# Kernel tuning notes

Measured on AMD Instinct MI355X. Metric: run time of the kernel, lower is better.

The kernel has to match this reference:

```python
import jax, jax.numpy as jnp
import numpy as np

D_MODEL, D_STATE, D_CONV, EXPAND = 1024, 16, 4, 2
D_INNER = EXPAND * D_MODEL
BATCH, L = 2, 2048


def setup_inputs() -> dict:
    key = jax.random.key(0)
    ks = jax.random.split(key, 8)
    s = lambda fan: 1.0 / float(np.sqrt(fan))
    x = jax.random.normal(ks[0], (BATCH, L, D_MODEL), jnp.float32)
    W_in = jax.random.normal(ks[1], (D_MODEL, 2 * D_INNER), jnp.float32) * s(D_MODEL)
    conv_w = jax.random.normal(ks[2], (D_INNER, 1, D_CONV), jnp.float32) * s(D_CONV)
    conv_b = jax.random.normal(ks[3], (D_INNER,), jnp.float32) * 0.1
    W_x = jax.random.normal(ks[4], (D_INNER, 2 * D_STATE + 1), jnp.float32) * s(D_INNER)
    w_dt = jax.random.normal(ks[5], (D_INNER,), jnp.float32)
    b_dt = jax.random.normal(ks[6], (D_INNER,), jnp.float32) * 0.1
    W_out = jax.random.normal(ks[7], (D_INNER, D_MODEL), jnp.float32) * s(D_INNER)
    A_log = jnp.log(jnp.broadcast_to(jnp.arange(1, D_STATE + 1, dtype=jnp.float32), (D_INNER, D_STATE)))
    Dp = jnp.ones((D_INNER,), jnp.float32)
    return dict(x=x, W_in=W_in, conv_w=conv_w, conv_b=conv_b, W_x=W_x,
                w_dt=w_dt, b_dt=b_dt, A_log=A_log, Dp=Dp, W_out=W_out)


def _silu(v):
    return v * jax.nn.sigmoid(v)


def _forward(x, W_in, conv_w, conv_b, W_x, w_dt, b_dt, A_log, Dp, W_out):
    xz = x @ W_in                                   # (B,L,2*Di)
    x_, z = jnp.split(xz, 2, axis=-1)               # (B,L,Di) each
    # causal depthwise conv over length (== torch pad d_conv-1 both sides then [:L])
    xc = jnp.transpose(x_, (0, 2, 1))               # (B,Di,L)
    xc = jax.lax.conv_general_dilated(
        xc, conv_w, window_strides=(1,), padding=[(D_CONV - 1, 0)],
        dimension_numbers=('NCH', 'OIH', 'NCH'), feature_group_count=D_INNER)
    xc = xc + conv_b[None, :, None]
    x_ = _silu(jnp.transpose(xc, (0, 2, 1)))        # (B,L,Di)

    bcd = x_ @ W_x                                  # (B,L,2N+1)
    B_ = bcd[..., :D_STATE]                         # (B,L,N)
    C = bcd[..., D_STATE:2 * D_STATE]               # (B,L,N)
    dt = jax.nn.softplus(bcd[..., -1:] * w_dt + b_dt)  # (B,L,Di)
    A = -jnp.exp(A_log)                             # (Di,N)

    def step(h, inp):
        dt_t, B_t, C_t, x_t = inp                   # (B,Di),(B,N),(B,N),(B,Di)
        dA = jnp.exp(dt_t[..., None] * A)           # (B,Di,N)
        h = dA * h + (dt_t * x_t)[..., None] * B_t[:, None, :]
        y = jnp.einsum('bdn,bn->bd', h, C_t)
        return h, y

    h0 = jnp.zeros((x.shape[0], D_INNER, D_STATE), x.dtype)
    xs = (jnp.transpose(dt, (1, 0, 2)), jnp.transpose(B_, (1, 0, 2)),
          jnp.transpose(C, (1, 0, 2)), jnp.transpose(x_, (1, 0, 2)))
    _, ys = jax.lax.scan(step, h0, xs)              # ys: (L,B,Di)
    y = jnp.transpose(ys, (1, 0, 2)) + x_ * Dp      # skip connection via D
    return (y * _silu(z)) @ W_out                   # (B,L,d_model)


def reference(x, W_in, conv_w, conv_b, W_x, w_dt, b_dt, A_log, Dp, W_out):
    return _forward(x, W_in, conv_w, conv_b, W_x, w_dt, b_dt, A_log, Dp, W_out)
```

## Files before the change

### kernel.cpp

```cpp
#include <hip/hip_runtime.h>
#include <hip/hip_bf16.h>
#include <stdint.h>

#define D_MODEL 1024
#define D_STATE 16
#define D_CONV  4
#define D_INNER 2048
#define BATCH   2
#define SEQLEN  2048
#define NROWS   (BATCH*SEQLEN)
#define BCD_LD  36
#define NCHUNK  32
#define CHUNKLEN (SEQLEN/NCHUNK)
#define KS2     16
#define L2E 1.44269504088896340f

typedef __attribute__((ext_vector_type(8))) short   short8;
typedef __attribute__((ext_vector_type(4))) float   f32x4;

__device__ __forceinline__ uint16_t f2bf(float f) {
    uint32_t u = __float_as_uint(f);
    return (uint16_t)((u + 0x7FFFu + ((u >> 16) & 1u)) >> 16);
}
__device__ __forceinline__ void gload16(const uint16_t* g, uint16_t* l) {
    __builtin_amdgcn_global_load_lds(
        (const __attribute__((address_space(1))) void*)g,
        (__attribute__((address_space(3))) void*)l, 16, 0, 0);
}
__device__ __forceinline__ void gload16f(const float* g, float* l) {
    __builtin_amdgcn_global_load_lds(
        (const __attribute__((address_space(1))) void*)g,
        (__attribute__((address_space(3))) void*)l, 16, 0, 0);
}
__device__ __forceinline__ float softplus_f(float v) {
    return fmaxf(v, 0.f) + __logf(1.f + __expf(-fabsf(v)));
}
__device__ __forceinline__ float silu_f(float v) {
    return v / (1.f + __expf(-v));
}
__device__ __forceinline__ short8 pack8(const float4 lo, const float4 hi) {
    short8 r;
    r[0] = (short)f2bf(lo.x); r[1] = (short)f2bf(lo.y);
    r[2] = (short)f2bf(lo.z); r[3] = (short)f2bf(lo.w);
    r[4] = (short)f2bf(hi.x); r[5] = (short)f2bf(hi.y);
    r[6] = (short)f2bf(hi.z); r[7] = (short)f2bf(hi.w);
    return r;
}

__global__ void kcvt(const float* __restrict__ in, uint16_t* __restrict__ out, int n4) {
    int T = blockIdx.x * 256 + threadIdx.x;
    if (T >= n4) return;
    const float4 v = *(const float4*)&in[(size_t)T * 4];
    ushort4 o;
    o.x = f2bf(v.x); o.y = f2bf(v.y); o.z = f2bf(v.z); o.w = f2bf(v.w);
    *(ushort4*)&out[(size_t)T * 4] = o;
}

__global__ void ktrans(const float* __restrict__ in, uint16_t* __restrict__ out,
                       int Kd, int Nd) {
    __shared__ float tile[32][33];
    const int n0 = blockIdx.x * 32, k0 = blockIdx.y * 32;
    const int tx = threadIdx.x & 31, ty = threadIdx.x >> 5;
#pragma unroll
    for (int i = 0; i < 4; ++i)
        tile[ty + i * 8][tx] = in[(size_t)(k0 + ty + i * 8) * Nd + n0 + tx];
    __syncthreads();
#pragma unroll
    for (int i = 0; i < 4; ++i)
        out[(size_t)(n0 + ty + i * 8) * Kd + k0 + tx] = f2bf(tile[tx][ty + i * 8]);
}

__global__ void kwxt(const float* __restrict__ Wx, float* __restrict__ Wxt) {
    const int T = blockIdx.x * 256 + threadIdx.x;
    const int j = T >> 11, k = T & 2047;
    Wxt[T] = (j < 33) ? Wx[(size_t)k * 33 + j] : 0.f;
}

template<int KDIM>
__global__ __launch_bounds__(256) void kgemm(const uint16_t* __restrict__ A,
                                             const uint16_t* __restrict__ B,
                                             float* __restrict__ C, const int ldc) {
    __shared__ uint16_t As[128 * 32];
    __shared__ uint16_t Bs[128 * 32];
    const int t = threadIdx.x;
    const int w = t >> 6, lane = t & 63;
    const int m0 = blockIdx.y * 128, n0 = blockIdx.x * 128;
    const int wm = (w >> 1) * 64, wn = (w & 1) * 64;
    f32x4 acc[4][4] = {};

    const int srow = t >> 2;
    const int scol = ((t & 3) ^ ((t >> 3) & 3)) * 8;
    const uint16_t* ga0 = A + (size_t)(m0 + srow) * KDIM + scol;
    const uint16_t* ga1 = A + (size_t)(m0 + 64 + srow) * KDIM + scol;
    const uint16_t* gb0 = B + (size_t)(n0 + srow) * KDIM + scol;
    const uint16_t* gb1 = B + (size_t)(n0 + 64 + srow) * KDIM + scol;
    uint16_t* lA0 = &As[w * 512];
    uint16_t* lA1 = &As[2048 + w * 512];
    uint16_t* lB0 = &Bs[w * 512];
    uint16_t* lB1 = &Bs[2048 + w * 512];

    const int fr = lane & 15, fg = (lane >> 4) * 8;
    const int psl = (((fg >> 3) ^ ((fr >> 1) & 3)) << 3);

    for (int kt = 0; kt < KDIM / 32; ++kt) {
        const int ko = kt * 32;
        gload16(ga0 + ko, lA0);
        gload16(ga1 + ko, lA1);
        gload16(gb0 + ko, lB0);
        gload16(gb1 + ko, lB1);
        __syncthreads();
        short8 a[4], b[4];
#pragma unroll
        for (int i = 0; i < 4; ++i) {
            a[i] = *(const short8*)&As[(wm + i * 16 + fr) * 32 + psl];
            b[i] = *(const short8*)&Bs[(wn + i * 16 + fr) * 32 + psl];
        }
#pragma unroll
        for (int i = 0; i < 4; ++i)
#pragma unroll
            for (int j = 0; j < 4; ++j)
                acc[i][j] = __builtin_amdgcn_mfma_f32_16x16x32_bf16(a[i], b[j], acc[i][j], 0, 0, 0);
        __syncthreads();
    }
    const int cr = (lane >> 4) * 4, cc = lane & 15;
#pragma unroll
    for (int i = 0; i < 4; ++i)
#pragma unroll
        for (int j = 0; j < 4; ++j)
#pragma unroll
            for (int r = 0; r < 4; ++r)
                C[(size_t)(m0 + wm + i * 16 + cr + r) * ldc + (n0 + wn + j * 16 + cc)] = acc[i][j][r];
}

template<int KDIM>
__global__ __launch_bounds__(256) void kgemm64(const uint16_t* __restrict__ A,
                                               const uint16_t* __restrict__ B,
                                               float* __restrict__ C, const int ldc) {
    __shared__ uint16_t As[64 * 32];
    __shared__ uint16_t Bs[128 * 32];
    const int t = threadIdx.x;
    const int w = t >> 6, lane = t & 63;
    const int m0 = blockIdx.y * 64, n0 = blockIdx.x * 128;
    const int wm = (w >> 1) * 32, wn = (w & 1) * 64;
    f32x4 acc[2][4] = {};

    const int srow = t >> 2;
    const int scol = ((t & 3) ^ ((t >> 3) & 3)) * 8;
    const uint16_t* ga0 = A + (size_t)(m0 + srow) * KDIM + scol;
    const uint16_t* gb0 = B + (size_t)(n0 + srow) * KDIM + scol;
    const uint16_t* gb1 = B + (size_t)(n0 + 64 + srow) * KDIM + scol;
    uint16_t* lA0 = &As[w * 512];
    uint16_t* lB0 = &Bs[w * 512];
    uint16_t* lB1 = &Bs[2048 + w * 512];

    const int fr = lane & 15, fg = (lane >> 4) * 8;
    const int psl = (((fg >> 3) ^ ((fr >> 1) & 3)) << 3);

    for (int kt = 0; kt < KDIM / 32; ++kt) {
        const int ko = kt * 32;
        gload16(ga0 + ko, lA0);
        gload16(gb0 + ko, lB0);
        gload16(gb1 + ko, lB1);
        __syncthreads();
        short8 a[2], b[4];
#pragma unroll
        for (int i = 0; i < 2; ++i)
            a[i] = *(const short8*)&As[(wm + i * 16 + fr) * 32 + psl];
#pragma unroll
        for (int j = 0; j < 4; ++j)
            b[j] = *(const short8*)&Bs[(wn + j * 16 + fr) * 32 + psl];
#pragma unroll
        for (int i = 0; i < 2; ++i)
#pragma unroll
            for (int j = 0; j < 4; ++j)
                acc[i][j] = __builtin_amdgcn_mfma_f32_16x16x32_bf16(a[i], b[j], acc[i][j], 0, 0, 0);
        __syncthreads();
    }
    const int cr = (lane >> 4) * 4, cc = lane & 15;
#pragma unroll
    for (int i = 0; i < 2; ++i)
#pragma unroll
        for (int j = 0; j < 4; ++j)
#pragma unroll
            for (int r = 0; r < 4; ++r)
                C[(size_t)(m0 + wm + i * 16 + cr + r) * ldc + (n0 + wn + j * 16 + cc)] = acc[i][j][r];
}

__global__ __launch_bounds__(256) void kgemm2m(const float* __restrict__ xs,
        const float* __restrict__ Wxt, float* __restrict__ part) {
    __shared__ float As[128 * 32];
    __shared__ float Bs[64 * 32];
    const int t = threadIdx.x;
    const int w = t >> 6, lane = t & 63;
    const int kb = blockIdx.x;
    const int m0 = blockIdx.y * 128;
    const int kc = kb * 128;
    f32x4 acc[2][3] = {};

    const int srow = t >> 3;
    const int scol = ((t & 7) ^ ((t >> 3) & 7)) * 4;
    float* lA[4]; float* lB[2];
#pragma unroll
    for (int r = 0; r < 4; ++r) lA[r] = &As[(r * 32 + w * 8) * 32];
#pragma unroll
    for (int r = 0; r < 2; ++r) lB[r] = &Bs[(r * 32 + w * 8) * 32];

    const int wm = w * 32;
    const int fr = lane & 15, fg = (lane >> 4) * 8;
    const int plo = (((fg >> 2) ^ (fr & 7))) * 4;
    const int phi = ((((fg >> 2) + 1) ^ (fr & 7))) * 4;

    for (int kt = 0; kt < 4; ++kt) {
        const int ko = kc + kt * 32;
#pragma unroll
        for (int r = 0; r < 4; ++r)
            gload16f(xs + (size_t)(m0 + r * 32 + srow) * 2048 + ko + scol, lA[r]);
#pragma unroll
        for (int r = 0; r < 2; ++r)
            gload16f(Wxt + (size_t)(r * 32 + srow) * 2048 + ko + scol, lB[r]);
        __syncthreads();
        short8 a[2], b[3];
#pragma unroll
        for (int i = 0; i < 2; ++i) {
            const float* base = &As[(wm + i * 16 + fr) * 32];
            a[i] = pack8(*(const float4*)&base[plo], *(const float4*)&base[phi]);
        }
#pragma unroll
        for (int j = 0; j < 3; ++j) {
            const float* base = &Bs[(j * 16 + fr) * 32];
            b[j] = pack8(*(const float4*)&base[plo], *(const float4*)&base[phi]);
        }
#pragma unroll
        for (int i = 0; i < 2; ++i)
#pragma unroll
            for (int j = 0; j < 3; ++j)
                acc[i][j] = __builtin_amdgcn_mfma_f32_16x16x32_bf16(a[i], b[j], acc[i][j], 0, 0, 0);
        __syncthreads();
    }
    const int cr = (lane >> 4) * 4, cc = lane & 15;
    float* pb = part + (size_t)kb * 4096 * 48;
#pragma unroll
    for (int i = 0; i < 2; ++i)
#pragma unroll
        for (int j = 0; j < 3; ++j)
#pragma unroll
            for (int r = 0; r < 4; ++r)
                pb[(size_t)(m0 + wm + i * 16 + cr + r) * 48 + j * 16 + cc] = acc[i][j][r];
}

__global__ void kred2(const float* __restrict__ part, float* __restrict__ bcd) {
    const int T = blockIdx.x * 256 + threadIdx.x;
    if (T >= 4096 * 48) return;
    const int row = T / 48, j = T - row * 48;
    if (j >= 33) return;
    float s = 0.f;
#pragma unroll
    for (int ks = 0; ks < KS2; ++ks) s += part[(size_t)ks * 4096 * 48 + T];
    bcd[(size_t)row * BCD_LD + j] = s;
}

__global__ void kdt(const float* __restrict__ bcd, const float* __restrict__ wdt,
                    const float* __restrict__ bdt, float* __restrict__ dtb) {
    const int T = blockIdx.x * 256 + threadIdx.x;
    const int row = T >> 9, dg = (T & 511) * 4;
    const float raw = bcd[(size_t)row * BCD_LD + 32];
    const float4 w = *(const float4*)&wdt[dg];
    const float4 b = *(const float4*)&bdt[dg];
    float4 o;
    o.x = softplus_f(raw * w.x + b.x);
    o.y = softplus_f(raw * w.y + b.y);
    o.z = softplus_f(raw * w.z + b.z);
    o.w = softplus_f(raw * w.w + b.w);
    *(float4*)&dtb[(size_t)row * 4096 + dg] = o;
}

__global__ __launch_bounds__(256) void kscan1(const float* __restrict__ xs,
        const float* __restrict__ bcd, const float* __restrict__ dtb,
        const float* __restrict__ Alog,
        float* __restrict__ hloc, float* __restrict__ sumdt) {
    const int T = blockIdx.x * 256 + threadIdx.x;
    const int sub = T & 3;
    const int ch = (T >> 2) & 4095;
    const int chunk = T >> 14;
    const int b = ch >> 11, d = ch & 2047;
    float Ae[4]; bool structured = true;
#pragma unroll
    for (int i = 0; i < 4; ++i) {
        const float a = __expf(Alog[d * 16 + sub * 4 + i]);
        Ae[i] = -a * L2E;
        structured = structured && (fabsf(a - (float)(sub * 4 + i + 1)) < 1e-3f);
    }
    float h0 = 0, h1 = 0, h2 = 0, h3 = 0, sdt = 0;
    const int row0 = b * SEQLEN + chunk * CHUNKLEN;
    if (structured) {
        for (int l0 = 0; l0 < CHUNKLEN; l0 += 4) {
            float dtv[4], xv[4]; float4 B4[4];
#pragma unroll
            for (int s = 0; s < 4; ++s) {
                const int row = row0 + l0 + s;
                dtv[s] = dtb[(size_t)row * 4096 + d];
                xv[s]  = xs[(size_t)row * D_INNER + d];
                B4[s]  = *(const float4*)&bcd[(size_t)row * BCD_LD + sub * 4];
            }
#pragma unroll
            for (int s = 0; s < 4; ++s) {
                const float e0 = __builtin_amdgcn_exp2f(dtv[s] * (-L2E));
                const float e2 = e0 * e0, e4 = e2 * e2, e8 = e4 * e4;
                const float bs = ((sub & 1) ? e4 : 1.f) * ((sub & 2) ? e8 : 1.f);
                const float d0 = bs * e0, d1 = d0 * e0, d2 = d1 * e0, d3 = d2 * e0;
                sdt += dtv[s];
                const float dtx = dtv[s] * xv[s];
                h0 = d0 * h0 + dtx * B4[s].x;
                h1 = d1 * h1 + dtx * B4[s].y;
                h2 = d2 * h2 + dtx * B4[s].z;
                h3 = d3 * h3 + dtx * B4[s].w;
            }
        }
    } else {
        for (int l0 = 0; l0 < CHUNKLEN; l0 += 4) {
            float dtv[4], xv[4]; float4 B4[4];
#pragma unroll
            for (int s = 0; s < 4; ++s) {
                const int row = row0 + l0 + s;
                dtv[s] = dtb[(size_t)row * 4096 + d];
                xv[s]  = xs[(size_t)row * D_INNER + d];
                B4[s]  = *(const float4*)&bcd[(size_t)row * BCD_LD + sub * 4];
            }
#pragma unroll
            for (int s = 0; s < 4; ++s) {
                sdt += dtv[s];
                const float dtx = dtv[s] * xv[s];
                h0 = __builtin_amdgcn_exp2f(dtv[s] * Ae[0]) * h0 + dtx * B4[s].x;
                h1 = __builtin_amdgcn_exp2f(dtv[s] * Ae[1]) * h1 + dtx * B4[s].y;
                h2 = __builtin_amdgcn_exp2f(dtv[s] * Ae[2]) * h2 + dtx * B4[s].z;
                h3 = __builtin_amdgcn_exp2f(dtv[s] * Ae[3]) * h3 + dtx * B4[s].w;
            }
        }
    }
    const int cc = chunk * 4096 + ch;
    *(float4*)&hloc[(size_t)cc * 16 + sub * 4] = make_float4(h0, h1, h2, h3);
    if (sub == 0) sumdt[cc] = sdt;
}

__global__ void kscan2(const float* __restrict__ hloc, const float* __restrict__ sumdt,
                       const float* __restrict__ Alog, float* __restrict__ h0buf) {
    const int T = blockIdx.x * 256 + threadIdx.x;
    const int n = T & 15, ch = T >> 4;
    const int d = ch & 2047;
    const float Ae = -__expf(Alog[d * 16 + n]) * L2E;
    float h = 0.f;
    for (int c = 0; c < NCHUNK; ++c) {
        const int cc = c * 4096 + ch;
        h0buf[(size_t)cc * 16 + n] = h;
        h = __builtin_amdgcn_exp2f(Ae * sumdt[cc]) * h + hloc[(size_t)cc * 16 + n];
    }
}

__global__ __launch_bounds__(256) void kscan3(const float* __restrict__ xs,
        const float* __restrict__ bcd, const float* __restrict__ dtb,
        const float* __restrict__ Alog,
        const float* __restrict__ Dp, const float* __restrict__ xz,
        const float* __restrict__ h0buf, uint16_t* __restrict__ u) {
    const int T = blockIdx.x * 256 + threadIdx.x;
    const int sub = T & 3;
    const int ch = (T >> 2) & 4095;
    const int chunk = T >> 14;
    const int b = ch >> 11, d = ch & 2047;
    float Ae[4]; bool structured = true;
#pragma unroll
    for (int i = 0; i < 4; ++i) {
        const float a = __expf(Alog[d * 16 + sub * 4 + i]);
        Ae[i] = -a * L2E;
        structured = structured && (fabsf(a - (float)(sub * 4 + i + 1)) < 1e-3f);
    }
    const float Dpd = Dp[d];
    const float4 hh = *(const float4*)&h0buf[(size_t)(chunk * 4096 + ch) * 16 + sub * 4];
    float h0 = hh.x, h1 = hh.y, h2 = hh.z, h3 = hh.w;
    const int row0 = b * SEQLEN + chunk * CHUNKLEN;
    if (structured) {
        for (int l0 = 0; l0 < CHUNKLEN; l0 += 4) {
            float dtv[4], xv[4], zv[4]; float4 B4[4], C4[4];
#pragma unroll
            for (int s = 0; s < 4; ++s) {
                const int row = row0 + l0 + s;
                dtv[s] = dtb[(size_t)row * 4096 + d];
                xv[s]  = xs[(size_t)row * D_INNER + d];
                B4[s]  = *(const float4*)&bcd[(size_t)row * BCD_LD + sub * 4];
                C4[s]  = *(const float4*)&bcd[(size_t)row * BCD_LD + 16 + sub * 4];
                if (sub == 0) zv[s] = xz[(size_t)row * 4096 + 2048 + d];
            }
#pragma unroll
            for (int s = 0; s < 4; ++s) {
                const int row = row0 + l0 + s;
                const float e0 = __builtin_amdgcn_exp2f(dtv[s] * (-L2E));
                const float e2 = e0 * e0, e4 = e2 * e2, e8 = e4 * e4;
                const float bs = ((sub & 1) ? e4 : 1.f) * ((sub & 2) ? e8 : 1.f);
                const float d0 = bs * e0, d1 = d0 * e0, d2 = d1 * e0, d3 = d2 * e0;
                const float dtx = dtv[s] * xv[s];
                h0 = d0 * h0 + dtx * B4[s].x;
                h1 = d1 * h1 + dtx * B4[s].y;
                h2 = d2 * h2 + dtx * B4[s].z;
                h3 = d3 * h3 + dtx * B4[s].w;
                float yp = h0 * C4[s].x + h1 * C4[s].y + h2 * C4[s].z + h3 * C4[s].w;
                yp += __shfl_xor(yp, 1);
                yp += __shfl_xor(yp, 2);
                if (sub == 0) {
                    const float uu = (yp + xv[s] * Dpd) * silu_f(zv[s]);
                    u[(size_t)row * D_INNER + d] = f2bf(uu);
                }
            }
        }
    } else {
        for (int l0 = 0; l0 < CHUNKLEN; l0 += 4) {
            float dtv[4], xv[4], zv[4]; float4 B4[4], C4[4];
#pragma unroll
            for (int s = 0; s < 4; ++s) {
                const int row = row0 + l0 + s;
                dtv[s] = dtb[(size_t)row * 4096 + d];
                xv[s]  = xs[(size_t)row * D_INNER + d];
                B4[s]  = *(const float4*)&bcd[(size_t)row * BCD_LD + sub * 4];
                C4[s]  = *(const float4*)&bcd[(size_t)row * BCD_LD + 16 + sub * 4];
                if (sub == 0) zv[s] = xz[(size_t)row * 4096 + 2048 + d];
            }
#pragma unroll
            for (int s = 0; s < 4; ++s) {
                const int row = row0 + l0 + s;
                const float dtx = dtv[s] * xv[s];
                h0 = __builtin_amdgcn_exp2f(dtv[s] * Ae[0]) * h0 + dtx * B4[s].x;
                h1 = __builtin_amdgcn_exp2f(dtv[s] * Ae[1]) * h1 + dtx * B4[s].y;
                h2 = __builtin_amdgcn_exp2f(dtv[s] * Ae[2]) * h2 + dtx * B4[s].z;
                h3 = __builtin_amdgcn_exp2f(dtv[s] * Ae[3]) * h3 + dtx * B4[s].w;
                float yp = h0 * C4[s].x + h1 * C4[s].y + h2 * C4[s].z + h3 * C4[s].w;
                yp += __shfl_xor(yp, 1);
                yp += __shfl_xor(yp, 2);
                if (sub == 0) {
                    const float uu = (yp + xv[s] * Dpd) * silu_f(zv[s]);
                    u[(size_t)row * D_INNER + d] = f2bf(uu);
                }
            }
        }
    }
}

__global__ void kconv(const float* __restrict__ xz, const float* __restrict__ cw,
                      const float* __restrict__ cb, float* __restrict__ xs) {
    size_t T = (size_t)blockIdx.x * 256 + threadIdx.x;
    int d = (int)(T & (D_INNER - 1));
    int row = (int)(T >> 11);
    int l = row & (SEQLEN - 1), b = row >> 11;
    const float4 w4 = *(const float4*)&cw[d * 4];
    float acc = cb[d];
    const size_t base = (size_t)b * SEQLEN;
    if (l >= 3) {
        acc += w4.x * xz[(base + l - 3) * 4096 + d];
        acc += w4.y * xz[(base + l - 2) * 4096 + d];
        acc += w4.z * xz[(base + l - 1) * 4096 + d];
        acc += w4.w * xz[(base + l    ) * 4096 + d];
    } else {
        if (l >= 2) acc += w4.y * xz[(base + l - 2) * 4096 + d];
        if (l >= 1) acc += w4.z * xz[(base + l - 1) * 4096 + d];
        acc += w4.w * xz[(base + l) * 4096 + d];
    }
    xs[T] = silu_f(acc);
}

extern "C" void kernel_launch(void* const* d_in, const int* in_sizes, int n_in,
                              void* d_out, int out_size, void* d_ws, size_t ws_size,
                              hipStream_t stream) {
    const float* x      = (const float*)d_in[0];
    const float* W_in   = (const float*)d_in[1];
    const float* conv_w = (const float*)d_in[2];
    const float* conv_b = (const float*)d_in[3];
    const float* W_x    = (const float*)d_in[4];
    const float* w_dt   = (const float*)d_in[5];
    const float* b_dt   = (const float*)d_in[6];
    const float* A_log  = (const float*)d_in[7];
    const float* Dp     = (const float*)d_in[8];
    const float* W_out  = (const float*)d_in[9];
    float* out = (float*)d_out;

    char* p = (char*)d_ws;
    uint16_t* xb  = (uint16_t*)p;  p += (size_t)NROWS * D_MODEL * 2;
    uint16_t* Wb  = (uint16_t*)p;  p += (size_t)4096 * 1024 * 2;
    uint16_t* Wob = (uint16_t*)p;  p += (size_t)1024 * 2048 * 2;
    float* xz     = (float*)p;     p += (size_t)NROWS * 4096 * 4;
    float* xs     = (float*)p;     p += (size_t)NROWS * D_INNER * 4;
    float* bcd    = (float*)p;     p += (size_t)NROWS * BCD_LD * 4;
    float* sumdt  = (float*)p;     p += (size_t)NCHUNK * 4096 * 4;
    float* Wxt    = (float*)p;     p += (size_t)64 * 2048 * 4;
    uint16_t* ub  = (uint16_t*)p;  p += (size_t)NROWS * D_INNER * 2;
    float* hloc   = (float*)xb;
    float* h0b    = (float*)Wb;
    float* part   = (float*)ub;
    float* dtb    = xz;

    kcvt<<<(NROWS * D_MODEL / 4 + 255) / 256, 256, 0, stream>>>(x, xb, NROWS * D_MODEL / 4);
    ktrans<<<dim3(4096 / 32, 1024 / 32), 256, 0, stream>>>(W_in, Wb, 1024, 4096);
    ktrans<<<dim3(1024 / 32, 2048 / 32), 256, 0, stream>>>(W_out, Wob, 2048, 1024);
    kwxt<<<(64 * 2048) / 256, 256, 0, stream>>>(W_x, Wxt);
    kgemm<1024><<<dim3(32, 32), 256, 0, stream>>>(xb, Wb, xz, 4096);
    kconv<<<NROWS * D_INNER / 256, 256, 0, stream>>>(xz, conv_w, conv_b, xs);
    kgemm2m<<<dim3(KS2, 32), 256, 0, stream>>>(xs, Wxt, part);
    kred2<<<(4096 * 48 + 255) / 256, 256, 0, stream>>>(part, bcd);
    kdt<<<(4096 * 512) / 256, 256, 0, stream>>>(bcd, w_dt, b_dt, dtb);
    kscan1<<<(4096 * 4 * NCHUNK) / 256, 256, 0, stream>>>(xs, bcd, dtb, A_log, hloc, sumdt);
    kscan2<<<(4096 * 16) / 256, 256, 0, stream>>>(hloc, sumdt, A_log, h0b);
    kscan3<<<(4096 * 4 * NCHUNK) / 256, 256, 0, stream>>>(xs, bcd, dtb, A_log, Dp, xz, h0b, ub);
    kgemm64<2048><<<dim3(1024 / 128, 4096 / 64), 256, 0, stream>>>(ub, Wob, out, 1024);
}
```

Before: 241.0 us.

## Pack dt/dtx and silu(z)/skip into bf16 pairs, restructure scan, swizzle GEMM grids

A new prep kernel precomputes softplus dt, dt*x, silu(z) and the D-skip term and packs each pair as two bf16 values into the existing xz buffer, so the scan kernels read one 32-bit word per row instead of several fp32 streams. The scan now uses 2 threads per channel with 8 states each instead of 4 with 4, doubles the chunk count, and kscan2 rewrites the chunk prefix states in place. Both GEMMs get an XCD-aware workgroup remap for better L2 locality. Storing dt and dt*x in bf16 lowers precision in the recurrence.

```diff
diff --git a/kernel.cpp b/kernel.cpp
--- a/kernel.cpp
+++ b/kernel.cpp
@@ -10,7 +10,7 @@
 #define SEQLEN  2048
 #define NROWS   (BATCH*SEQLEN)
 #define BCD_LD  36
-#define NCHUNK  32
+#define NCHUNK  64
 #define CHUNKLEN (SEQLEN/NCHUNK)
 #define KS2     16
 #define L2E 1.44269504088896340f
@@ -21,6 +21,9 @@
 __device__ __forceinline__ uint16_t f2bf(float f) {
     uint32_t u = __float_as_uint(f);
     return (uint16_t)((u + 0x7FFFu + ((u >> 16) & 1u)) >> 16);
+}
+__device__ __forceinline__ uint32_t pack2bf(float lo, float hi) {
+    return (uint32_t)f2bf(lo) | ((uint32_t)f2bf(hi) << 16);
 }
 __device__ __forceinline__ void gload16(const uint16_t* g, uint16_t* l) {
     __builtin_amdgcn_global_load_lds(
@@ -76,7 +79,7 @@
     Wxt[T] = (j < 33) ? Wx[(size_t)k * 33 + j] : 0.f;
 }
 
-template<int KDIM>
+template<int KDIM, int GXL>
 __global__ __launch_bounds__(256) void kgemm(const uint16_t* __restrict__ A,
                                              const uint16_t* __restrict__ B,
                                              float* __restrict__ C, const int ldc) {
@@ -84,7 +87,9 @@
     __shared__ uint16_t Bs[128 * 32];
     const int t = threadIdx.x;
     const int w = t >> 6, lane = t & 63;
-    const int m0 = blockIdx.y * 128, n0 = blockIdx.x * 128;
+    int wg = blockIdx.y * (1 << GXL) + blockIdx.x;
+    wg = (wg & 7) * ((gridDim.x * gridDim.y) >> 3) + (wg >> 3);
+    const int m0 = (wg >> GXL) * 128, n0 = (wg & ((1 << GXL) - 1)) * 128;
     const int wm = (w >> 1) * 64, wn = (w & 1) * 64;
     f32x4 acc[4][4] = {};
 
@@ -132,7 +137,7 @@
                 C[(size_t)(m0 + wm + i * 16 + cr + r) * ldc + (n0 + wn + j * 16 + cc)] = acc[i][j][r];
 }
 
-template<int KDIM>
+template<int KDIM, int GXL>
 __global__ __launch_bounds__(256) void kgemm64(const uint16_t* __restrict__ A,
                                                const uint16_t* __restrict__ B,
                                                float* __restrict__ C, const int ldc) {
@@ -140,7 +145,9 @@
     __shared__ uint16_t Bs[128 * 32];
     const int t = threadIdx.x;
     const int w = t >> 6, lane = t & 63;
-    const int m0 = blockIdx.y * 64, n0 = blockIdx.x * 128;
+    int wg = blockIdx.y * (1 << GXL) + blockIdx.x;
+    wg = (wg & 7) * ((gridDim.x * gridDim.y) >> 3) + (wg >> 3);
+    const int m0 = (wg >> GXL) * 64, n0 = (wg & ((1 << GXL) - 1)) * 128;
     const int wm = (w >> 1) * 32, wn = (w & 1) * 64;
     f32x4 acc[2][4] = {};
 
@@ -259,185 +266,232 @@
     bcd[(size_t)row * BCD_LD + j] = s;
 }
 
-__global__ void kdt(const float* __restrict__ bcd, const float* __restrict__ wdt,
-                    const float* __restrict__ bdt, float* __restrict__ dtb) {
+__global__ void kprep(const float* __restrict__ bcd, const float* __restrict__ wdt,
+                      const float* __restrict__ bdt, const float* __restrict__ Dp,
+                      const float* __restrict__ xs, float* __restrict__ xz) {
     const int T = blockIdx.x * 256 + threadIdx.x;
     const int row = T >> 9, dg = (T & 511) * 4;
     const float raw = bcd[(size_t)row * BCD_LD + 32];
-    const float4 w = *(const float4*)&wdt[dg];
-    const float4 b = *(const float4*)&bdt[dg];
-    float4 o;
-    o.x = softplus_f(raw * w.x + b.x);
-    o.y = softplus_f(raw * w.y + b.y);
-    o.z = softplus_f(raw * w.z + b.z);
-    o.w = softplus_f(raw * w.w + b.w);
-    *(float4*)&dtb[(size_t)row * 4096 + dg] = o;
-}
-
-__global__ __launch_bounds__(256) void kscan1(const float* __restrict__ xs,
-        const float* __restrict__ bcd, const float* __restrict__ dtb,
-        const float* __restrict__ Alog,
-        float* __restrict__ hloc, float* __restrict__ sumdt) {
+    const float4 w  = *(const float4*)&wdt[dg];
+    const float4 b  = *(const float4*)&bdt[dg];
+    const float4 Dv = *(const float4*)&Dp[dg];
+    const float4 xv = *(const float4*)&xs[(size_t)row * D_INNER + dg];
+    const float4 zv = *(const float4*)&xz[(size_t)row * 4096 + 2048 + dg];
+    const float dt0 = softplus_f(raw * w.x + b.x);
+    const float dt1 = softplus_f(raw * w.y + b.y);
+    const float dt2 = softplus_f(raw * w.z + b.z);
+    const float dt3 = softplus_f(raw * w.w + b.w);
+    uint4 pd, ps;
+    pd.x = pack2bf(dt0, dt0 * xv.x);
+    pd.y = pack2bf(dt1, dt1 * xv.y);
+    pd.z = pack2bf(dt2, dt2 * xv.z);
+    pd.w = pack2bf(dt3, dt3 * xv.w);
+    const float s0 = silu_f(zv.x), s1 = silu_f(zv.y), s2 = silu_f(zv.z), s3 = silu_f(zv.w);
+    ps.x = pack2bf(s0, xv.x * Dv.x * s0);
+    ps.y = pack2bf(s1, xv.y * Dv.y * s1);
+    ps.z = pack2bf(s2, xv.z * Dv.z * s2);
+    ps.w = pack2bf(s3, xv.w * Dv.w * s3);
+    uint32_t* xzu = (uint32_t*)xz;
+    *(uint4*)&xzu[(size_t)row * 4096 + dg] = pd;
+    *(uint4*)&xzu[(size_t)row * 4096 + 2048 + dg] = ps;
+}
+
+__global__ __launch_bounds__(256) void kscan1(const uint32_t* __restrict__ dtdx,
+        const float* __restrict__ bcd, const float* __restrict__ Alog,
+        float* __restrict__ hbuf, float* __restrict__ sumdt) {
     const int T = blockIdx.x * 256 + threadIdx.x;
-    const int sub = T & 3;
-    const int ch = (T >> 2) & 4095;
-    const int chunk = T >> 14;
+    const int sub = T & 1;
+    const int ch  = (T >> 1) & 4095;
+    const int chunk = T >> 13;
     const int b = ch >> 11, d = ch & 2047;
-    float Ae[4]; bool structured = true;
-#pragma unroll
-    for (int i = 0; i < 4; ++i) {
-        const float a = __expf(Alog[d * 16 + sub * 4 + i]);
+    float Ae[8]; bool st = true;
+#pragma unroll
+    for (int i = 0; i < 8; ++i) {
+        const float a = __expf(Alog[d * 16 + sub * 8 + i]);
         Ae[i] = -a * L2E;
-        structured = structured && (fabsf(a - (float)(sub * 4 + i + 1)) < 1e-3f);
-    }
-    float h0 = 0, h1 = 0, h2 = 0, h3 = 0, sdt = 0;
+        st = st && (fabsf(a - (float)(sub * 8 + i + 1)) < 1e-3f);
+    }
+    float h[8] = {};
+    float sdt = 0.f;
     const int row0 = b * SEQLEN + chunk * CHUNKLEN;
-    if (structured) {
-        for (int l0 = 0; l0 < CHUNKLEN; l0 += 4) {
-            float dtv[4], xv[4]; float4 B4[4];
-#pragma unroll
-            for (int s = 0; s < 4; ++s) {
-                const int row = row0 + l0 + s;
-                dtv[s] = dtb[(size_t)row * 4096 + d];
-                xv[s]  = xs[(size_t)row * D_INNER + d];
-                B4[s]  = *(const float4*)&bcd[(size_t)row * BCD_LD + sub * 4];
-            }
-#pragma unroll
-            for (int s = 0; s < 4; ++s) {
-                const float e0 = __builtin_amdgcn_exp2f(dtv[s] * (-L2E));
+    const uint32_t* pD = dtdx + (size_t)row0 * 4096 + d;
+    const float* pB = bcd + (size_t)row0 * BCD_LD + sub * 8;
+    if (st) {
+        for (int l0 = 0; l0 < CHUNKLEN; l0 += 2) {
+            uint32_t pk[2]; float4 B0[2], B1[2];
+#pragma unroll
+            for (int s = 0; s < 2; ++s) {
+                pk[s] = pD[(size_t)s * 4096];
+                B0[s] = *(const float4*)(pB + s * BCD_LD);
+                B1[s] = *(const float4*)(pB + s * BCD_LD + 4);
+            }
+#pragma unroll
+            for (int s = 0; s < 2; ++s) {
+                const float dt  = __uint_as_float(pk[s] << 16);
+                const float dtx = __uint_as_float(pk[s] & 0xffff0000u);
+                sdt += dt;
+                const float e0 = __builtin_amdgcn_exp2f(dt * (-L2E));
                 const float e2 = e0 * e0, e4 = e2 * e2, e8 = e4 * e4;
-                const float bs = ((sub & 1) ? e4 : 1.f) * ((sub & 2) ? e8 : 1.f);
-                const float d0 = bs * e0, d1 = d0 * e0, d2 = d1 * e0, d3 = d2 * e0;
-                sdt += dtv[s];
-                const float dtx = dtv[s] * xv[s];
-                h0 = d0 * h0 + dtx * B4[s].x;
-                h1 = d1 * h1 + dtx * B4[s].y;
-                h2 = d2 * h2 + dtx * B4[s].z;
-                h3 = d3 * h3 + dtx * B4[s].w;
-            }
+                float dec = sub ? e8 : 1.f;
+                dec *= e0; h[0] = fmaf(dec, h[0], dtx * B0[s].x);
+                dec *= e0; h[1] = fmaf(dec, h[1], dtx * B0[s].y);
+                dec *= e0; h[2] = fmaf(dec, h[2], dtx * B0[s].z);
+                dec *= e0; h[3] = fmaf(dec, h[3], dtx * B0[s].w);
+                dec *= e0; h[4] = fmaf(dec, h[4], dtx * B1[s].x);
+                dec *= e0; h[5] = fmaf(dec, h[5], dtx * B1[s].y);
+                dec *= e0; h[6] = fmaf(dec, h[6], dtx * B1[s].z);
+                dec *= e0; h[7] = fmaf(dec, h[7], dtx * B1[s].w);
+            }
+            pD += 2 * 4096; pB += 2 * BCD_LD;
         }
     } else {
-        for (int l0 = 0; l0 < CHUNKLEN; l0 += 4) {
-            float dtv[4], xv[4]; float4 B4[4];
-#pragma unroll
-            for (int s = 0; s < 4; ++s) {
-                const int row = row0 + l0 + s;
-                dtv[s] = dtb[(size_t)row * 4096 + d];
-                xv[s]  = xs[(size_t)row * D_INNER + d];
-                B4[s]  = *(const float4*)&bcd[(size_t)row * BCD_LD + sub * 4];
-            }
-#pragma unroll
-            for (int s = 0; s < 4; ++s) {
-                sdt += dtv[s];
-                const float dtx = dtv[s] * xv[s];
-                h0 = __builtin_amdgcn_exp2f(dtv[s] * Ae[0]) * h0 + dtx * B4[s].x;
-                h1 = __builtin_amdgcn_exp2f(dtv[s] * Ae[1]) * h1 + dtx * B4[s].y;
-                h2 = __builtin_amdgcn_exp2f(dtv[s] * Ae[2]) * h2 + dtx * B4[s].z;
-                h3 = __builtin_amdgcn_exp2f(dtv[s] * Ae[3]) * h3 + dtx * B4[s].w;
-            }
-        }
-    }
-    const int cc = chunk * 4096 + ch;
-    *(float4*)&hloc[(size_t)cc * 16 + sub * 4] = make_float4(h0, h1, h2, h3);
-    if (sub == 0) sumdt[cc] = sdt;
-}
-
-__global__ void kscan2(const float* __restrict__ hloc, const float* __restrict__ sumdt,
-                       const float* __restrict__ Alog, float* __restrict__ h0buf) {
+        for (int l0 = 0; l0 < CHUNKLEN; l0 += 2) {
+            uint32_t pk[2]; float4 B0[2], B1[2];
+#pragma unroll
+            for (int s = 0; s < 2; ++s) {
+                pk[s] = pD[(size_t)s * 4096];
+                B0[s] = *(const float4*)(pB + s * BCD_LD);
+                B1[s] = *(const float4*)(pB + s * BCD_LD + 4);
+            }
+#pragma unroll
+            for (int s = 0; s < 2; ++s) {
+                const float dt  = __uint_as_float(pk[s] << 16);
+                const float dtx = __uint_as_float(pk[s] & 0xffff0000u);
+                sdt += dt;
+                h[0] = fmaf(__builtin_amdgcn_exp2f(dt * Ae[0]), h[0], dtx * B0[s].x);
+                h[1] = fmaf(__builtin_amdgcn_exp2f(dt * Ae[1]), h[1], dtx * B0[s].y);
+                h[2] = fmaf(__builtin_amdgcn_exp2f(dt * Ae[2]), h[2], dtx * B0[s].z);
+                h[3] = fmaf(__builtin_amdgcn_exp2f(dt * Ae[3]), h[3], dtx * B0[s].w);
+                h[4] = fmaf(__builtin_amdgcn_exp2f(dt * Ae[4]), h[4], dtx * B1[s].x);
+                h[5] = fmaf(__builtin_amdgcn_exp2f(dt * Ae[5]), h[5], dtx * B1[s].y);
+                h[6] = fmaf(__builtin_amdgcn_exp2f(dt * Ae[6]), h[6], dtx * B1[s].z);
+                h[7] = fmaf(__builtin_amdgcn_exp2f(dt * Ae[7]), h[7], dtx * B1[s].w);
+            }
+            pD += 2 * 4096; pB += 2 * BCD_LD;
+        }
+    }
+    const size_t cc = (size_t)(chunk * 4096 + ch) * 16 + sub * 8;
+    *(float4*)&hbuf[cc]     = make_float4(h[0], h[1], h[2], h[3]);
+    *(float4*)&hbuf[cc + 4] = make_float4(h[4], h[5], h[6], h[7]);
+    if (sub == 0) sumdt[chunk * 4096 + ch] = sdt;
+}
+
+__global__ void kscan2(float* __restrict__ hbuf, const float* __restrict__ sumdt,
+                       const float* __restrict__ Alog) {
     const int T = blockIdx.x * 256 + threadIdx.x;
     const int n = T & 15, ch = T >> 4;
     const int d = ch & 2047;
     const float Ae = -__expf(Alog[d * 16 + n]) * L2E;
     float h = 0.f;
     for (int c = 0; c < NCHUNK; ++c) {
-        const int cc = c * 4096 + ch;
-        h0buf[(size_t)cc * 16 + n] = h;
-        h = __builtin_amdgcn_exp2f(Ae * sumdt[cc]) * h + hloc[(size_t)cc * 16 + n];
-    }
-}
-
-__global__ __launch_bounds__(256) void kscan3(const float* __restrict__ xs,
-        const float* __restrict__ bcd, const float* __restrict__ dtb,
-        const float* __restrict__ Alog,
-        const float* __restrict__ Dp, const float* __restrict__ xz,
-        const float* __restrict__ h0buf, uint16_t* __restrict__ u) {
+        const size_t idx = (size_t)(c * 4096 + ch) * 16 + n;
+        const float loc = hbuf[idx];
+        hbuf[idx] = h;
+        h = __builtin_amdgcn_exp2f(Ae * sumdt[c * 4096 + ch]) * h + loc;
+    }
+}
+
+__global__ __launch_bounds__(256) void kscan3(const uint32_t* __restrict__ dtdx,
+        const float* __restrict__ bcd, const float* __restrict__ Alog,
+        const uint32_t* __restrict__ szw, const float* __restrict__ hbuf,
+        uint16_t* __restrict__ u) {
     const int T = blockIdx.x * 256 + threadIdx.x;
-    const int sub = T & 3;
-    const int ch = (T >> 2) & 4095;
-    const int chunk = T >> 14;
+    const int sub = T & 1;
+    const int ch  = (T >> 1) & 4095;
+    const int chunk = T >> 13;
     const int b = ch >> 11, d = ch & 2047;
-    float Ae[4]; bool structured = true;
-#pragma unroll
-    for (int i = 0; i < 4; ++i) {
-        const float a = __expf(Alog[d * 16 + sub * 4 + i]);
+    float Ae[8]; bool st = true;
+#pragma unroll
+    for (int i = 0; i < 8; ++i) {
+        const float a = __expf(Alog[d * 16 + sub * 8 + i]);
         Ae[i] = -a * L2E;
-        structured = structured && (fabsf(a - (float)(sub * 4 + i + 1)) < 1e-3f);
-    }
-    const float Dpd = Dp[d];
-    const float4 hh = *(const float4*)&h0buf[(size_t)(chunk * 4096 + ch) * 16 + sub * 4];
-    float h0 = hh.x, h1 = hh.y, h2 = hh.z, h3 = hh.w;
+        st = st && (fabsf(a - (float)(sub * 8 + i + 1)) < 1e-3f);
+    }
+    float h[8];
+    {
+        const size_t cc = (size_t)(chunk * 4096 + ch) * 16 + sub * 8;
+        const float4 h0 = *(const float4*)&hbuf[cc];
+        const float4 h1 = *(const float4*)&hbuf[cc + 4];
+        h[0] = h0.x; h[1] = h0.y; h[2] = h0.z; h[3] = h0.w;
+        h[4] = h1.x; h[5] = h1.y; h[6] = h1.z; h[7] = h1.w;
+    }
     const int row0 = b * SEQLEN + chunk * CHUNKLEN;
-    if (structured) {
-        for (int l0 = 0; l0 < CHUNKLEN; l0 += 4) {
-            float dtv[4], xv[4], zv[4]; float4 B4[4], C4[4];
-#pragma unroll
-            for (int s = 0; s < 4; ++s) {
-                const int row = row0 + l0 + s;
-                dtv[s] = dtb[(size_t)row * 4096 + d];
-                xv[s]  = xs[(size_t)row * D_INNER + d];
-                B4[s]  = *(const float4*)&bcd[(size_t)row * BCD_LD + sub * 4];
-                C4[s]  = *(const float4*)&bcd[(size_t)row * BCD_LD + 16 + sub * 4];
-                if (sub == 0) zv[s] = xz[(size_t)row * 4096 + 2048 + d];
-            }
-#pragma unroll
-            for (int s = 0; s < 4; ++s) {
-                const int row = row0 + l0 + s;
-                const float e0 = __builtin_amdgcn_exp2f(dtv[s] * (-L2E));
+    const uint32_t* pD = dtdx + (size_t)row0 * 4096 + d;
+    const uint32_t* pS = szw  + (size_t)row0 * 4096 + d;
+    const float* pB = bcd + (size_t)row0 * BCD_LD + sub * 8;
+    uint16_t* pU = u + (size_t)row0 * D_INNER + d;
+    if (st) {
+        for (int l0 = 0; l0 < CHUNKLEN; l0 += 2) {
+            uint32_t pk[2], qk[2]; float4 B0[2], B1[2], C0[2], C1[2];
+#pragma unroll
+            for (int s = 0; s < 2; ++s) {
+                pk[s] = pD[(size_t)s * 4096];
+                B0[s] = *(const float4*)(pB + s * BCD_LD);
+                B1[s] = *(const float4*)(pB + s * BCD_LD + 4);
+                C0[s] = *(const float4*)(pB + s * BCD_LD + 16);
+                C1[s] = *(const float4*)(pB + s * BCD_LD + 20);
+                if (sub == 0) qk[s] = pS[(size_t)s * 4096];
+            }
+#pragma unroll
+            for (int s = 0; s < 2; ++s) {
+                const float dt  = __uint_as_float(pk[s] << 16);
+                const float dtx = __uint_as_float(pk[s] & 0xffff0000u);
+                const float e0 = __builtin_amdgcn_exp2f(dt * (-L2E));
                 const float e2 = e0 * e0, e4 = e2 * e2, e8 = e4 * e4;
-                const float bs = ((sub & 1) ? e4 : 1.f) * ((sub & 2) ? e8 : 1.f);
-                const float d0 = bs * e0, d1 = d0 * e0, d2 = d1 * e0, d3 = d2 * e0;
-                const float dtx = dtv[s] * xv[s];
-                h0 = d0 * h0 + dtx * B4[s].x;
-                h1 = d1 * h1 + dtx * B4[s].y;
-                h2 = d2 * h2 + dtx * B4[s].z;
-                h3 = d3 * h3 + dtx * B4[s].w;
-                float yp = h0 * C4[s].x + h1 * C4[s].y + h2 * C4[s].z + h3 * C4[s].w;
-                yp += __shfl_xor(yp, 1);
-                yp += __shfl_xor(yp, 2);
+                float dec = sub ? e8 : 1.f;
+                dec *= e0; h[0] = fmaf(dec, h[0], dtx * B0[s].x);
+                dec *= e0; h[1] = fmaf(dec, h[1], dtx * B0[s].y);
+                dec *= e0; h[2] = fmaf(dec, h[2], dtx * B0[s].z);
+                dec *= e0; h[3] = fmaf(dec, h[3], dtx * B0[s].w);
+                dec *= e0; h[4] = fmaf(dec, h[4], dtx * B1[s].x);
+                dec *= e0; h[5] = fmaf(dec, h[5], dtx * B1[s].y);
+                dec *= e0; h[6] = fmaf(dec, h[6], dtx * B1[s].z);
+                dec *= e0; h[7] = fmaf(dec, h[7], dtx * B1[s].w);
+                float y = h[0] * C0[s].x + h[1] * C0[s].y + h[2] * C0[s].z + h[3] * C0[s].w
+                        + h[4] * C1[s].x + h[5] * C1[s].y + h[6] * C1[s].z + h[7] * C1[s].w;
+                y += __shfl_xor(y, 1);
                 if (sub == 0) {
-                    const float uu = (yp + xv[s] * Dpd) * silu_f(zv[s]);
-                    u[(size_t)row * D_INNER + d] = f2bf(uu);
+                    const float sz = __uint_as_float(qk[s] << 16);
+                    const float w2 = __uint_as_float(qk[s] & 0xffff0000u);
+                    pU[(size_t)s * D_INNER] = f2bf(fmaf(y, sz, w2));
                 }
             }
+            pD += 2 * 4096; pS += 2 * 4096; pB += 2 * BCD_LD; pU += 2 * D_INNER;
         }
     } else {
-        for (int l0 = 0; l0 < CHUNKLEN; l0 += 4) {
-            float dtv[4], xv[4], zv[4]; float4 B4[4], C4[4];
-#pragma unroll
-            for (int s = 0; s < 4; ++s) {
-                const int row = row0 + l0 + s;
-                dtv[s] = dtb[(size_t)row * 4096 + d];
-                xv[s]  = xs[(size_t)row * D_INNER + d];
-                B4[s]  = *(const float4*)&bcd[(size_t)row * BCD_LD + sub * 4];
-                C4[s]  = *(const float4*)&bcd[(size_t)row * BCD_LD + 16 + sub * 4];
-                if (sub == 0) zv[s] = xz[(size_t)row * 4096 + 2048 + d];
-            }
-#pragma unroll
-            for (int s = 0; s < 4; ++s) {
-                const int row = row0 + l0 + s;
-                const float dtx = dtv[s] * xv[s];
-                h0 = __builtin_amdgcn_exp2f(dtv[s] * Ae[0]) * h0 + dtx * B4[s].x;
-                h1 = __builtin_amdgcn_exp2f(dtv[s] * Ae[1]) * h1 + dtx * B4[s].y;
-                h2 = __builtin_amdgcn_exp2f(dtv[s] * Ae[2]) * h2 + dtx * B4[s].z;
-                h3 = __builtin_amdgcn_exp2f(dtv[s] * Ae[3]) * h3 + dtx * B4[s].w;
-                float yp = h0 * C4[s].x + h1 * C4[s].y + h2 * C4[s].z + h3 * C4[s].w;
-                yp += __shfl_xor(yp, 1);
-                yp += __shfl_xor(yp, 2);
+        for (int l0 = 0; l0 < CHUNKLEN; l0 += 2) {
+            uint32_t pk[2], qk[2]; float4 B0[2], B1[2], C0[2], C1[2];
+#pragma unroll
+            for (int s = 0; s < 2; ++s) {
+                pk[s] = pD[(size_t)s * 4096];
+                B0[s] = *(const float4*)(pB + s * BCD_LD);
+                B1[s] = *(const float4*)(pB + s * BCD_LD + 4);
+                C0[s] = *(const float4*)(pB + s * BCD_LD + 16);
+                C1[s] = *(const float4*)(pB + s * BCD_LD + 20);
+                if (sub == 0) qk[s] = pS[(size_t)s * 4096];
+            }
+#pragma unroll
+            for (int s = 0; s < 2; ++s) {
+                const float dt  = __uint_as_float(pk[s] << 16);
+                const float dtx = __uint_as_float(pk[s] & 0xffff0000u);
+                h[0] = fmaf(__builtin_amdgcn_exp2f(dt * Ae[0]), h[0], dtx * B0[s].x);
+                h[1] = fmaf(__builtin_amdgcn_exp2f(dt * Ae[1]), h[1], dtx * B0[s].y);
+                h[2] = fmaf(__builtin_amdgcn_exp2f(dt * Ae[2]), h[2], dtx * B0[s].z);
+                h[3] = fmaf(__builtin_amdgcn_exp2f(dt * Ae[3]), h[3], dtx * B0[s].w);
+                h[4] = fmaf(__builtin_amdgcn_exp2f(dt * Ae[4]), h[4], dtx * B1[s].x);
+                h[5] = fmaf(__builtin_amdgcn_exp2f(dt * Ae[5]), h[5], dtx * B1[s].y);
+                h[6] = fmaf(__builtin_amdgcn_exp2f(dt * Ae[6]), h[6], dtx * B1[s].z);
+                h[7] = fmaf(__builtin_amdgcn_exp2f(dt * Ae[7]), h[7], dtx * B1[s].w);
+                float y = h[0] * C0[s].x + h[1] * C0[s].y + h[2] * C0[s].z + h[3] * C0[s].w
+                        + h[4] * C1[s].x + h[5] * C1[s].y + h[6] * C1[s].z + h[7] * C1[s].w;
+                y += __shfl_xor(y, 1);
                 if (sub == 0) {
-                    const float uu = (yp + xv[s] * Dpd) * silu_f(zv[s]);
-                    u[(size_t)row * D_INNER + d] = f2bf(uu);
+                    const float sz = __uint_as_float(qk[s] << 16);
+                    const float w2 = __uint_as_float(qk[s] & 0xffff0000u);
+                    pU[(size_t)s * D_INNER] = f2bf(fmaf(y, sz, w2));
                 }
             }
+            pD += 2 * 4096; pS += 2 * 4096; pB += 2 * BCD_LD; pU += 2 * D_INNER;
         }
     }
 }
@@ -489,22 +543,22 @@
     float* sumdt  = (float*)p;     p += (size_t)NCHUNK * 4096 * 4;
     float* Wxt    = (float*)p;     p += (size_t)64 * 2048 * 4;
     uint16_t* ub  = (uint16_t*)p;  p += (size_t)NROWS * D_INNER * 2;
-    float* hloc   = (float*)xb;
-    float* h0b    = (float*)Wb;
+    float* hbuf   = (float*)xb;
     float* part   = (float*)ub;
-    float* dtb    = xz;
+    uint32_t* dtdx = (uint32_t*)xz;
+    uint32_t* szw  = (uint32_t*)xz + 2048;
 
     kcvt<<<(NROWS * D_MODEL / 4 + 255) / 256, 256, 0, stream>>>(x, xb, NROWS * D_MODEL / 4);
     ktrans<<<dim3(4096 / 32, 1024 / 32), 256, 0, stream>>>(W_in, Wb, 1024, 4096);
     ktrans<<<dim3(1024 / 32, 2048 / 32), 256, 0, stream>>>(W_out, Wob, 2048, 1024);
     kwxt<<<(64 * 2048) / 256, 256, 0, stream>>>(W_x, Wxt);
-    kgemm<1024><<<dim3(32, 32), 256, 0, stream>>>(xb, Wb, xz, 4096);
+    kgemm<1024, 5><<<dim3(32, 32), 256, 0, stream>>>(xb, Wb, xz, 4096);
     kconv<<<NROWS * D_INNER / 256, 256, 0, stream>>>(xz, conv_w, conv_b, xs);
     kgemm2m<<<dim3(KS2, 32), 256, 0, stream>>>(xs, Wxt, part);
     kred2<<<(4096 * 48 + 255) / 256, 256, 0, stream>>>(part, bcd);
-    kdt<<<(4096 * 512) / 256, 256, 0, stream>>>(bcd, w_dt, b_dt, dtb);
-    kscan1<<<(4096 * 4 * NCHUNK) / 256, 256, 0, stream>>>(xs, bcd, dtb, A_log, hloc, sumdt);
-    kscan2<<<(4096 * 16) / 256, 256, 0, stream>>>(hloc, sumdt, A_log, h0b);
-    kscan3<<<(4096 * 4 * NCHUNK) / 256, 256, 0, stream>>>(xs, bcd, dtb, A_log, Dp, xz, h0b, ub);
-    kgemm64<2048><<<dim3(1024 / 128, 4096 / 64), 256, 0, stream>>>(ub, Wob, out, 1024);
-}
+    kprep<<<(4096 * 512) / 256, 256, 0, stream>>>(bcd, w_dt, b_dt, Dp, xs, xz);
+    kscan1<<<(4096 * 2 * NCHUNK) / 256, 256, 0, stream>>>(dtdx, bcd, A_log, hbuf, sumdt);
+    kscan2<<<(4096 * 16) / 256, 256, 0, stream>>>(hbuf, sumdt, A_log);
+    kscan3<<<(4096 * 2 * NCHUNK) / 256, 256, 0, stream>>>(dtdx, bcd, A_log, szw, hbuf, ub);
+    kgemm64<2048, 3><<<dim3(1024 / 128, 4096 / 64), 256, 0, stream>>>(ub, Wob, out, 1024);
+}
```

New measurement: 240.8 us. No clear change (-0.1%).
